# Optimization experiments

Hardware: AMD Instinct MI355X
Metric: run time of the kernel (lower is better)

Reference implementation:

```python
import jax, jax.numpy as jnp
import numpy as np

TAU = 1.0

def setup_inputs() -> dict:
    key = jax.random.key(0)
    scores = jax.random.normal(key, (16, 2048), dtype=jnp.float32)
    return {"scores": scores}

def reference(scores):
    # scores: [B, n]
    B, n = scores.shape
    # row-sum of pairwise abs differences: Asum[b,i] = sum_k |s_i - s_k|
    Asum = jnp.sum(jnp.abs(scores[:, :, None] - scores[:, None, :]), axis=-1)  # [B, n]
    # scaling[j] = n + 1 - 2*(j+1)
    scaling = (n + 1 - 2 * (jnp.arange(n, dtype=jnp.float32) + 1.0))  # [n]
    # P_max[b, j, i] = s[b,i] * scaling[j] - Asum[b,i]
    P_max = scores[:, None, :] * scaling[None, :, None] - Asum[:, None, :]  # [B, n, n]
    P_hat = jax.nn.softmax(P_max / TAU, axis=-1)
    return P_hat
```

## Files before the change

### kernel.cpp

```cpp
#include <hip/hip_runtime.h>
#include <hip/hip_bf16.h>

#define N 2048
#define B 16
#define LOG2E 1.44269504088896340736f

typedef float v4f __attribute__((ext_vector_type(4)));

__global__ __launch_bounds__(256) void asum_kernel(const float* __restrict__ s,
                                                   float* __restrict__ asum2) {
    const int b = blockIdx.y;
    const int chunk = blockIdx.x;

    __shared__ float row[N];
    __shared__ float partial[256];
    const v4f* g4 = (const v4f*)(s + b * N);
    v4f* r4 = (v4f*)row;
    r4[threadIdx.x] = g4[threadIdx.x];
    r4[threadIdx.x + 256] = g4[threadIdx.x + 256];
    __syncthreads();

    const int il = threadIdx.x & 127;
    const int half = threadIdx.x >> 7;
    const int i = chunk * 128 + il;
    const float si = row[i];
    const v4f* row4 = (const v4f*)(row + half * (N / 2));
    float acc = 0.0f;
#pragma unroll 4
    for (int k = 0; k < N / 8; ++k) {
        v4f rv = row4[k];
        acc += fabsf(si - rv.x) + fabsf(si - rv.y) +
               fabsf(si - rv.z) + fabsf(si - rv.w);
    }
    partial[threadIdx.x] = acc;
    __syncthreads();
    if (threadIdx.x < 128)
        asum2[b * N + i] = LOG2E * (partial[threadIdx.x] + partial[threadIdx.x + 128]);
}

__global__ __launch_bounds__(256) void softmax_rows(const float* __restrict__ s,
                                                    const float* __restrict__ asum2,
                                                    float* __restrict__ out) {
    __shared__ float ls[N];
    __shared__ float la[N];

    const int t = threadIdx.x;
    const int lane = t & 63;
    const int wave = t >> 6;
    const int b = blockIdx.y;
    const int j = blockIdx.x * 4 + wave;

    {
        const v4f* g4 = (const v4f*)(s + (size_t)b * N);
        const v4f* ga4 = (const v4f*)(asum2 + (size_t)b * N);
        v4f* l4 = (v4f*)ls;
        v4f* m4 = (v4f*)la;
        v4f s0 = g4[t], s1 = g4[t + 256];
        v4f a0 = ga4[t], a1 = ga4[t + 256];
        s0 *= LOG2E; s1 *= LOG2E;
        l4[t] = s0; l4[t + 256] = s1;
        m4[t] = a0; m4[t + 256] = a1;
    }
    __syncthreads();

    const float cj = (float)(N - 1 - 2 * j);

    const v4f* ls4 = (const v4f*)ls;
    const v4f* la4 = (const v4f*)la;

    float v[32];
#pragma unroll
    for (int c = 0; c < 8; ++c) {
        v4f sv = ls4[c * 64 + lane];
        v4f av = la4[c * 64 + lane];
        v[c * 4 + 0] = sv.x * cj - av.x;
        v[c * 4 + 1] = sv.y * cj - av.y;
        v[c * 4 + 2] = sv.z * cj - av.z;
        v[c * 4 + 3] = sv.w * cj - av.w;
    }

    float m = v[0];
#pragma unroll
    for (int i = 1; i < 32; ++i) m = fmaxf(m, v[i]);
#pragma unroll
    for (int off = 32; off >= 1; off >>= 1)
        m = fmaxf(m, __shfl_xor(m, off));

    float sum = 0.0f;
#pragma unroll
    for (int i = 0; i < 32; ++i) {
        v[i] = __builtin_amdgcn_exp2f(v[i] - m);
        sum += v[i];
    }
#pragma unroll
    for (int off = 32; off >= 1; off >>= 1)
        sum += __shfl_xor(sum, off);

    const float r = 1.0f / sum;

    v4f* o4 = (v4f*)(out + ((size_t)b * N + j) * N);
#pragma unroll
    for (int c = 0; c < 8; ++c) {
        v4f o;
        o.x = v[c * 4 + 0] * r;
        o.y = v[c * 4 + 1] * r;
        o.z = v[c * 4 + 2] * r;
        o.w = v[c * 4 + 3] * r;
        __builtin_nontemporal_store(o, &o4[c * 64 + lane]);
    }
}

extern "C" void kernel_launch(void* const* d_in, const int* in_sizes, int n_in,
                              void* d_out, int out_size, void* d_ws, size_t ws_size,
                              hipStream_t stream) {
    const float* scores = (const float*)d_in[0];
    float* out = (float*)d_out;
    float* asum2 = (float*)d_ws;

    dim3 g1(N / 128, B);
    asum_kernel<<<g1, 256, 0, stream>>>(scores, asum2);

    dim3 g2(N / 4, B);
    softmax_rows<<<g2, 256, 0, stream>>>(scores, asum2, out);
}
```

Measured before the change: 272.0 us.

## Process four softmax rows per wave to amortize shared-memory staging

Each wave now computes four output rows instead of one, so every block covers 16 rows and the grid shrinks fourfold. The per-block loads of scores and Asum into shared memory, and the LDS reads, are reused across more rows. Max and sum reductions are restructured into trees with interleaved shuffles for more ILP. Nontemporal stores are replaced with plain stores. The cost is higher register pressure (128 floats of row values per thread), which may lower occupancy on a kernel that is bound by its 256MB of output writes.

Result: faster. 263.4 us (-3.2%).

```diff
diff --git a/kernel.cpp b/kernel.cpp
--- a/kernel.cpp
+++ b/kernel.cpp
@@ -48,7 +48,7 @@
     const int lane = t & 63;
     const int wave = t >> 6;
     const int b = blockIdx.y;
-    const int j = blockIdx.x * 4 + wave;
+    const int j0 = blockIdx.x * 16 + wave;
 
     {
         const v4f* g4 = (const v4f*)(s + (size_t)b * N);
@@ -63,50 +63,80 @@
     }
     __syncthreads();
 
-    const float cj = (float)(N - 1 - 2 * j);
+    float c[4];
+#pragma unroll
+    for (int r = 0; r < 4; ++r)
+        c[r] = (float)(N - 1 - 2 * (j0 + 4 * r));
 
     const v4f* ls4 = (const v4f*)ls;
     const v4f* la4 = (const v4f*)la;
 
-    float v[32];
+    float v[4][32];
 #pragma unroll
-    for (int c = 0; c < 8; ++c) {
-        v4f sv = ls4[c * 64 + lane];
-        v4f av = la4[c * 64 + lane];
-        v[c * 4 + 0] = sv.x * cj - av.x;
-        v[c * 4 + 1] = sv.y * cj - av.y;
-        v[c * 4 + 2] = sv.z * cj - av.z;
-        v[c * 4 + 3] = sv.w * cj - av.w;
+    for (int ch = 0; ch < 8; ++ch) {
+        v4f sv = ls4[ch * 64 + lane];
+        v4f av = la4[ch * 64 + lane];
+#pragma unroll
+        for (int r = 0; r < 4; ++r) {
+            v[r][ch * 4 + 0] = sv.x * c[r] - av.x;
+            v[r][ch * 4 + 1] = sv.y * c[r] - av.y;
+            v[r][ch * 4 + 2] = sv.z * c[r] - av.z;
+            v[r][ch * 4 + 3] = sv.w * c[r] - av.w;
+        }
     }
 
-    float m = v[0];
+    float m[4];
 #pragma unroll
-    for (int i = 1; i < 32; ++i) m = fmaxf(m, v[i]);
+    for (int r = 0; r < 4; ++r) {
+        float t16[16];
 #pragma unroll
-    for (int off = 32; off >= 1; off >>= 1)
-        m = fmaxf(m, __shfl_xor(m, off));
-
-    float sum = 0.0f;
+        for (int i = 0; i < 16; ++i) t16[i] = fmaxf(v[r][i], v[r][i + 16]);
 #pragma unroll
-    for (int i = 0; i < 32; ++i) {
-        v[i] = __builtin_amdgcn_exp2f(v[i] - m);
-        sum += v[i];
+        for (int i = 0; i < 8; ++i) t16[i] = fmaxf(t16[i], t16[i + 8]);
+#pragma unroll
+        for (int i = 0; i < 4; ++i) t16[i] = fmaxf(t16[i], t16[i + 4]);
+        m[r] = fmaxf(fmaxf(t16[0], t16[1]), fmaxf(t16[2], t16[3]));
     }
 #pragma unroll
-    for (int off = 32; off >= 1; off >>= 1)
-        sum += __shfl_xor(sum, off);
+    for (int off = 32; off >= 1; off >>= 1) {
+#pragma unroll
+        for (int r = 0; r < 4; ++r)
+            m[r] = fmaxf(m[r], __shfl_xor(m[r], off));
+    }
 
-    const float r = 1.0f / sum;
+    float sum[4];
+#pragma unroll
+    for (int r = 0; r < 4; ++r) {
+        float p0 = 0.0f, p1 = 0.0f, p2 = 0.0f, p3 = 0.0f;
+#pragma unroll
+        for (int i = 0; i < 32; i += 4) {
+            v[r][i + 0] = __builtin_amdgcn_exp2f(v[r][i + 0] - m[r]); p0 += v[r][i + 0];
+            v[r][i + 1] = __builtin_amdgcn_exp2f(v[r][i + 1] - m[r]); p1 += v[r][i + 1];
+            v[r][i + 2] = __builtin_amdgcn_exp2f(v[r][i + 2] - m[r]); p2 += v[r][i + 2];
+            v[r][i + 3] = __builtin_amdgcn_exp2f(v[r][i + 3] - m[r]); p3 += v[r][i + 3];
+        }
+        sum[r] = (p0 + p1) + (p2 + p3);
+    }
+#pragma unroll
+    for (int off = 32; off >= 1; off >>= 1) {
+#pragma unroll
+        for (int r = 0; r < 4; ++r)
+            sum[r] += __shfl_xor(sum[r], off);
+    }
 
-    v4f* o4 = (v4f*)(out + ((size_t)b * N + j) * N);
 #pragma unroll
-    for (int c = 0; c < 8; ++c) {
-        v4f o;
-        o.x = v[c * 4 + 0] * r;
-        o.y = v[c * 4 + 1] * r;
-        o.z = v[c * 4 + 2] * r;
-        o.w = v[c * 4 + 3] * r;
-        __builtin_nontemporal_store(o, &o4[c * 64 + lane]);
+    for (int r = 0; r < 4; ++r) {
+        const float rz = 1.0f / sum[r];
+        v4f* o4 = (v4f*)(out + ((size_t)b * N + (j0 + 4 * r)) * N);
+#pragma unroll
+        for (int ch = 0; ch < 8; ++ch) {
+            v4f o;
+            o.x = v[r][ch * 4 + 0] * rz;
+            o.y = v[r][ch * 4 + 1] * rz;
+            o.z = v[r][ch * 4 + 2] * rz;
+            o.w = v[r][ch * 4 + 3] * rz;
+            o4[ch * 64 + lane] = o;
+        }
     }
 }
 
@@ -120,6 +150,6 @@
     dim3 g1(N / 128, B);
     asum_kernel<<<g1, 256, 0, stream>>>(scores, asum2);
 
-    dim3 g2(N / 4, B);
+    dim3 g2(N / 16, B);
     softmax_rows<<<g2, 256, 0, stream>>>(scores, asum2, out);
 }
```
